# Optimization experiments

Measured on AMD Instinct MI355X. Metric: run time of the kernel, lower is better.

The kernel has to match this reference:

```python
import jax, jax.numpy as jnp
import numpy as np

B = 1024      # batch
D = 512       # input/output dim per module
H = 1024      # expert hidden dim
T = 8         # num_tasks
NTE = 2       # experts per task
NSE = 2       # shared experts
E = T * NTE + NSE   # 18 experts per layer
# expert_input_idx: each expert reads the module it belongs to (tasks 0..7, shared=8)
EXPERT_IDX = np.array([m for m in range(T + 1) for _ in range(2)])  # [E]


def _lin_init(k, shape, fan_in):
    s = 1.0 / np.sqrt(fan_in)
    return jax.random.uniform(k, shape, jnp.float32, -s, s)


def setup_inputs() -> dict:
    key = jax.random.key(0)
    ks = jax.random.split(key, 20)
    inp = {"inputs": jax.random.normal(ks[0], (B, T + 1, D), jnp.float32)}
    # layer 0: experts D->H->D (stacked over E), gates for M=9 modules
    inp["W1_0"] = _lin_init(ks[1], (E, D, H), D)
    inp["b1_0"] = _lin_init(ks[2], (E, H), D)
    inp["W2_0"] = _lin_init(ks[3], (E, H, D), H)
    inp["b2_0"] = _lin_init(ks[4], (E, D), H)
    inp["Wg_0"] = _lin_init(ks[5], (T + 1, D, E), D)
    inp["bg_0"] = _lin_init(ks[6], (T + 1, E), D)
    # layer 1 (final): gates only for M=T modules
    inp["W1_1"] = _lin_init(ks[7], (E, D, H), D)
    inp["b1_1"] = _lin_init(ks[8], (E, H), D)
    inp["W2_1"] = _lin_init(ks[9], (E, H, D), H)
    inp["b2_1"] = _lin_init(ks[10], (E, D), H)
    inp["Wg_1"] = _lin_init(ks[11], (T, D, E), D)
    inp["bg_1"] = _lin_init(ks[12], (T, E), D)
    # self-exp residual weights: per task [L=2, NTE], shared [L-1=1, NSE]
    sc = 1.0 / np.sqrt(NTE)
    inp["sew_task"] = jax.random.uniform(ks[13], (T, 2, NTE), jnp.float32, -sc, sc)
    inp["sew_shared"] = jax.random.uniform(ks[14], (1, NSE), jnp.float32, -sc, sc)
    return inp


def _build_add(rows):
    # rows: list of [2]-vectors, one per fully-active module; block-diagonal layout
    M = len(rows)
    add = jnp.zeros((M, E), jnp.float32)
    for m, w in enumerate(rows):
        add = add.at[m, 2 * m:2 * m + 2].set(w)
    return add


def _layer(x, W1, b1, W2, b2, Wg, bg, add):
    # x: [B, M_in, D]; experts share input of their owning module
    xe = x[:, EXPERT_IDX, :]                                   # [B, E, D]
    h = jax.nn.relu(jnp.einsum('bed,edh->beh', xe, W1) + b1)   # [B, E, H]
    eo = jnp.einsum('beh,eho->beo', h, W2) + b2                # [B, E, D]
    M = Wg.shape[0]
    g = jax.nn.softmax(jnp.einsum('bmd,mde->bme', x[:, :M, :], Wg) + bg, axis=-1)
    g = g + add[None]                                          # self-exp residual
    return jnp.einsum('bme,beo->bmo', g, eo)                   # [B, M, D]


def reference(inputs, W1_0, b1_0, W2_0, b2_0, Wg_0, bg_0,
              W1_1, b1_1, W2_1, b2_1, Wg_1, bg_1, sew_task, sew_shared):
    add0 = _build_add([sew_task[t, 0] for t in range(T)] + [sew_shared[0]])  # [T+1, E]
    add1 = _build_add([sew_task[t, 1] for t in range(T)])                    # [T, E]
    x = _layer(inputs, W1_0, b1_0, W2_0, b2_0, Wg_0, bg_0, add0)  # [B, T+1, D]
    x = _layer(x, W1_1, b1_1, W2_1, b2_1, Wg_1, bg_1, add1)       # [B, T, D]
    return x
```

## Files before the change

kernel.cpp:

```cpp
#include <hip/hip_runtime.h>

typedef unsigned short u16;
typedef unsigned int u32;
typedef __attribute__((ext_vector_type(8))) short short8;
typedef __attribute__((ext_vector_type(4))) float floatx4;

#define GLOAD_LDS16(gp, lp)                                                              \
  __builtin_amdgcn_global_load_lds((const __attribute__((address_space(1))) void*)(gp),  \
                                   (__attribute__((address_space(3))) void*)(lp), 16, 0, 0)

__device__ __forceinline__ u16 f2bf(float f) {
  u32 u = __float_as_uint(f);
  u += 0x7fffu + ((u >> 16) & 1u);
  return (u16)(u >> 16);
}

__device__ __forceinline__ void bf8_to_f(const u16* p, float* o) {
  const uint4 v = *(const uint4*)p;
  const u32 a[4] = {v.x, v.y, v.z, v.w};
#pragma unroll
  for (int i = 0; i < 4; i++) {
    o[2 * i]     = __uint_as_float(a[i] << 16);
    o[2 * i + 1] = __uint_as_float(a[i] & 0xffff0000u);
  }
}

__global__ __launch_bounds__(256) void wtrans_kernel(const float* __restrict__ W,
                                                     u16* __restrict__ WT,
                                                     int K, int N) {
  __shared__ float tile[64][65];
  const int t = threadIdx.x;
  const int e = blockIdx.z;
  const int n0 = blockIdx.x * 64;
  const int k0 = blockIdx.y * 64;
  const float* Wp = W + ((size_t)e * K + k0) * N + n0;
  const int r = t >> 4;
  const int c = (t & 15) << 2;
#pragma unroll
  for (int p = 0; p < 4; p++) {
    const int row = r + p * 16;
    const float4 v = *(const float4*)(Wp + (size_t)row * N + c);
    tile[row][c + 0] = v.x; tile[row][c + 1] = v.y;
    tile[row][c + 2] = v.z; tile[row][c + 3] = v.w;
  }
  __syncthreads();
  u16* WTp = WT + ((size_t)e * N + n0) * K + k0;
#pragma unroll
  for (int p = 0; p < 4; p++) {
    const int row = r + p * 16;
    u32 lo = (u32)f2bf(tile[c + 0][row]) | ((u32)f2bf(tile[c + 1][row]) << 16);
    u32 hi = (u32)f2bf(tile[c + 2][row]) | ((u32)f2bf(tile[c + 3][row]) << 16);
    *(uint2*)(WTp + (size_t)row * K + c) = make_uint2(lo, hi);
  }
}

__global__ __launch_bounds__(256) void wgtrans_kernel(const float* __restrict__ Wg,
                                                      u16* __restrict__ WgT, int total) {
  int idx = blockIdx.x * 256 + threadIdx.x;
  if (idx >= total) return;
  int d = idx & 511;
  int r = idx >> 9;
  int e = r % 18;
  int m = r / 18;
  WgT[idx] = f2bf(Wg[((size_t)(m * 512 + d)) * 18 + e]);
}

__global__ __launch_bounds__(256) void cvtbf_kernel(const float* __restrict__ src,
                                                    u16* __restrict__ dst, int n4) {
  int i = blockIdx.x * 256 + threadIdx.x;
  if (i >= n4) return;
  float4 v = ((const float4*)src)[i];
  u32 lo = (u32)f2bf(v.x) | ((u32)f2bf(v.y) << 16);
  u32 hi = (u32)f2bf(v.z) | ((u32)f2bf(v.w) << 16);
  ((uint2*)dst)[i] = make_uint2(lo, hi);
}

template <bool RELU_BF16_OUT>
__global__ __launch_bounds__(256, 3) void gemm_kernel(
    const u16* __restrict__ A, const u16* __restrict__ BT,
    const float* __restrict__ bias, void* __restrict__ Cout,
    int lda, int a_shift, int a_mul, int ldc, int c_mul, int N, int K) {
  __shared__ __align__(16) u16 As[128 * 64];
  __shared__ __align__(16) u16 Bs[128 * 64];

  const int tid = threadIdx.x;
  const int lane = tid & 63;
  const int wave = tid >> 6;
  const int e = blockIdx.y;
  const int mt = blockIdx.x & 7;
  const int nt = blockIdx.x >> 3;
  const int m0 = mt << 7, n0 = nt << 7;

  const u16* Aexp = A + (size_t)((e >> a_shift) * a_mul);
  const u16* Bexp = BT + (size_t)e * (size_t)N * (size_t)K;

  const int colsw = (((lane & 7) ^ ((lane >> 3) & 7)) << 3);
  const u16* aptr[4];
  const u16* bptr[4];
  u16* lA[4];
  u16* lB[4];
#pragma unroll
  for (int i = 0; i < 4; i++) {
    const int cch = wave * 4 + i;
    const int row = cch * 8 + (lane >> 3);
    aptr[i] = Aexp + (size_t)(m0 + row) * lda + colsw;
    bptr[i] = Bexp + (size_t)(n0 + row) * K + colsw;
    lA[i] = As + cch * 512;
    lB[i] = Bs + cch * 512;
  }

  floatx4 acc[4][4];
#pragma unroll
  for (int i = 0; i < 4; i++)
#pragma unroll
    for (int j = 0; j < 4; j++) acc[i][j] = (floatx4){0.f, 0.f, 0.f, 0.f};

  const int wm = (wave & 1) << 6;
  const int wn = (wave >> 1) << 6;
  const int r15 = lane & 15;
  const int quad = lane >> 4;

  int aoff[4], boff[4];
#pragma unroll
  for (int i = 0; i < 4; i++) {
    const int ra = wm + i * 16 + r15;
    aoff[i] = ra * 64 + ((quad ^ (ra & 7)) << 3);
    const int rb = wn + i * 16 + r15;
    boff[i] = rb * 64 + ((quad ^ (rb & 7)) << 3);
  }

  for (int k0 = 0; k0 < K; k0 += 64) {
    __syncthreads();
#pragma unroll
    for (int i = 0; i < 4; i++) GLOAD_LDS16(aptr[i] + k0, lA[i]);
#pragma unroll
    for (int i = 0; i < 4; i++) GLOAD_LDS16(bptr[i] + k0, lB[i]);
    __syncthreads();
#pragma unroll
    for (int s = 0; s < 2; s++) {
      short8 af[4], bfr[4];
#pragma unroll
      for (int i = 0; i < 4; i++) af[i] = *(const short8*)(As + (aoff[i] ^ (s << 5)));
#pragma unroll
      for (int j = 0; j < 4; j++) bfr[j] = *(const short8*)(Bs + (boff[j] ^ (s << 5)));
#pragma unroll
      for (int i = 0; i < 4; i++)
#pragma unroll
        for (int j = 0; j < 4; j++)
          acc[i][j] = __builtin_amdgcn_mfma_f32_16x16x32_bf16(af[i], bfr[j], acc[i][j], 0, 0, 0);
    }
  }

  const int ccol0 = n0 + wn + r15;
  const int crow0 = m0 + wm + quad * 4;
  float bv[4];
#pragma unroll
  for (int j = 0; j < 4; j++) bv[j] = bias[e * N + ccol0 + j * 16];

  if constexpr (RELU_BF16_OUT) {
    u16* Co = (u16*)Cout + (size_t)e * c_mul;
#pragma unroll
    for (int i = 0; i < 4; i++)
#pragma unroll
      for (int r = 0; r < 4; r++) {
        const size_t rowoff = (size_t)(crow0 + i * 16 + r) * ldc;
#pragma unroll
        for (int j = 0; j < 4; j++) {
          float v = acc[i][j][r] + bv[j];
          v = v > 0.f ? v : 0.f;
          Co[rowoff + ccol0 + j * 16] = f2bf(v);
        }
      }
  } else {
    float* Co = (float*)Cout + (size_t)e * c_mul;
#pragma unroll
    for (int i = 0; i < 4; i++)
#pragma unroll
      for (int r = 0; r < 4; r++) {
        const size_t rowoff = (size_t)(crow0 + i * 16 + r) * ldc;
#pragma unroll
        for (int j = 0; j < 4; j++) Co[rowoff + ccol0 + j * 16] = acc[i][j][r] + bv[j];
      }
  }
}

template <int M, int LAYER>
__global__ __launch_bounds__(256) void gating_kernel(
    const u16* __restrict__ xbf, const u16* __restrict__ WgT,
    const float* __restrict__ bg, const float* __restrict__ sew_task,
    const float* __restrict__ sew_shared, float* __restrict__ wsm) {
  const int lane = threadIdx.x & 63;
  const int wave = threadIdx.x >> 6;
  const int m = blockIdx.y;
  const int b0 = blockIdx.x * 8 + wave * 2;

  float xa[8], xb[8];
  bf8_to_f(xbf + (size_t)b0 * 4608 + m * 512 + lane * 8, xa);
  bf8_to_f(xbf + (size_t)(b0 + 1) * 4608 + m * 512 + lane * 8, xb);

  float lg0[18], lg1[18];
#pragma unroll
  for (int e = 0; e < 18; e++) {
    float w[8];
    bf8_to_f(WgT + ((size_t)m * 18 + e) * 512 + lane * 8, w);
    float s0 = 0.f, s1 = 0.f;
#pragma unroll
    for (int i = 0; i < 8; i++) { s0 = fmaf(w[i], xa[i], s0); s1 = fmaf(w[i], xb[i], s1); }
#pragma unroll
    for (int off = 1; off < 64; off <<= 1) {
      s0 += __shfl_xor(s0, off, 64);
      s1 += __shfl_xor(s1, off, 64);
    }
    const float bgv = bg[m * 18 + e];
    lg0[e] = s0 + bgv;
    lg1[e] = s1 + bgv;
  }
  float mx0 = lg0[0], mx1 = lg1[0];
#pragma unroll
  for (int e = 1; e < 18; e++) { mx0 = fmaxf(mx0, lg0[e]); mx1 = fmaxf(mx1, lg1[e]); }
  float sum0 = 0.f, sum1 = 0.f;
#pragma unroll
  for (int e = 0; e < 18; e++) { sum0 += __expf(lg0[e] - mx0); sum1 += __expf(lg1[e] - mx1); }
  float my0 = lg0[0], my1 = lg1[0];
#pragma unroll
  for (int e = 1; e < 18; e++)
    if (lane == e) { my0 = lg0[e]; my1 = lg1[e]; }
  float w0 = __expf(my0 - mx0) / sum0;
  float w1 = __expf(my1 - mx1) / sum1;
  if ((lane >> 1) == m) {
    float add;
    if (M == 9 && m == 8) add = sew_shared[lane & 1];
    else                  add = sew_task[m * 4 + 2 * LAYER + (lane & 1)];
    w0 += add; w1 += add;
  }
  if (lane < 18) {
    wsm[((size_t)b0 * M + m) * 18 + lane] = w0;
    wsm[((size_t)(b0 + 1) * M + m) * 18 + lane] = w1;
  }
}

template <int M, bool BF16OUT>
__global__ __launch_bounds__(256) void wsum_kernel(
    const float* __restrict__ eo, const float* __restrict__ wsm,
    float* __restrict__ outf, u16* __restrict__ outb) {
  __shared__ float ws[2 * M * 18];
  const int t = threadIdx.x;
  const int b0 = blockIdx.x * 2;
  for (int i = t; i < 2 * M * 18; i += 256) ws[i] = wsm[(size_t)b0 * M * 18 + i];
  __syncthreads();
  const int lb = t >> 7;
  const int s = t & 127;
  const int b = b0 + lb;
  const float* eob = eo + (size_t)b * 9216 + s * 4;
  const float* wr = ws + lb * M * 18;

  float4 acc[M];
#pragma unroll
  for (int m = 0; m < M; m++) acc[m] = make_float4(0.f, 0.f, 0.f, 0.f);
#pragma unroll
  for (int e = 0; e < 18; e++) {
    const float4 v = *(const float4*)(eob + e * 512);
#pragma unroll
    for (int m = 0; m < M; m++) {
      const float w = wr[m * 18 + e];
      acc[m].x = fmaf(w, v.x, acc[m].x);
      acc[m].y = fmaf(w, v.y, acc[m].y);
      acc[m].z = fmaf(w, v.z, acc[m].z);
      acc[m].w = fmaf(w, v.w, acc[m].w);
    }
  }
  if constexpr (BF16OUT) {
    u16* ob = outb + (size_t)b * 4608 + s * 4;
#pragma unroll
    for (int m = 0; m < M; m++) {
      u32 lo = (u32)f2bf(acc[m].x) | ((u32)f2bf(acc[m].y) << 16);
      u32 hi = (u32)f2bf(acc[m].z) | ((u32)f2bf(acc[m].w) << 16);
      *(uint2*)(ob + m * 512) = make_uint2(lo, hi);
    }
  } else {
    float* ob = outf + (size_t)b * (M * 512) + s * 4;
#pragma unroll
    for (int m = 0; m < M; m++) *(float4*)(ob + m * 512) = acc[m];
  }
}

extern "C" void kernel_launch(void* const* d_in, const int* in_sizes, int n_in,
                              void* d_out, int out_size, void* d_ws, size_t ws_size,
                              hipStream_t stream) {
  const float* x0   = (const float*)d_in[0];
  const float* W1_0 = (const float*)d_in[1];
  const float* b1_0 = (const float*)d_in[2];
  const float* W2_0 = (const float*)d_in[3];
  const float* b2_0 = (const float*)d_in[4];
  const float* Wg_0 = (const float*)d_in[5];
  const float* bg_0 = (const float*)d_in[6];
  const float* W1_1 = (const float*)d_in[7];
  const float* b1_1 = (const float*)d_in[8];
  const float* W2_1 = (const float*)d_in[9];
  const float* b2_1 = (const float*)d_in[10];
  const float* Wg_1 = (const float*)d_in[11];
  const float* bg_1 = (const float*)d_in[12];
  const float* sewt = (const float*)d_in[13];
  const float* sews = (const float*)d_in[14];
  float* out = (float*)d_out;

  char* p = (char*)d_ws;
  auto take = [&](size_t n) { char* r = p; p += (n + 255) & ~(size_t)255; return r; };
  u16*   x0bf = (u16*)take(4718592ull * 2);
  u16*   W1T0 = (u16*)take(9437184ull * 2);
  u16*   W2T0 = (u16*)take(9437184ull * 2);
  u16*   W1T1 = (u16*)take(9437184ull * 2);
  u16*   W2T1 = (u16*)take(9437184ull * 2);
  u16*   WgT0 = (u16*)take(82944ull * 2);
  u16*   WgT1 = (u16*)take(73728ull * 2);
  u16*   hbf  = (u16*)take(18874368ull * 2);
  float* eo   = (float*)take(9437184ull * 4);
  u16*   x1bf = (u16*)take(4718592ull * 2);
  float* wsm0 = (float*)take(165888ull * 4);
  float* wsm1 = (float*)take(147456ull * 4);

  dim3 blk(256);
  wtrans_kernel<<<dim3(16, 8, 18), blk, 0, stream>>>(W1_0, W1T0, 512, 1024);
  wtrans_kernel<<<dim3(8, 16, 18), blk, 0, stream>>>(W2_0, W2T0, 1024, 512);
  wtrans_kernel<<<dim3(16, 8, 18), blk, 0, stream>>>(W1_1, W1T1, 512, 1024);
  wtrans_kernel<<<dim3(8, 16, 18), blk, 0, stream>>>(W2_1, W2T1, 1024, 512);
  wgtrans_kernel<<<dim3(324), blk, 0, stream>>>(Wg_0, WgT0, 82944);
  wgtrans_kernel<<<dim3(288), blk, 0, stream>>>(Wg_1, WgT1, 73728);
  cvtbf_kernel<<<dim3(4608), blk, 0, stream>>>(x0, x0bf, 1179648);

  gating_kernel<9, 0><<<dim3(128, 9), blk, 0, stream>>>(x0bf, WgT0, bg_0, sewt, sews, wsm0);
  gemm_kernel<true><<<dim3(64, 18), blk, 0, stream>>>(
      x0bf, W1T0, b1_0, (void*)hbf, 4608, 1, 512, 18432, 1024, 1024, 512);
  gemm_kernel<false><<<dim3(32, 18), blk, 0, stream>>>(
      hbf, W2T0, b2_0, (void*)eo, 18432, 0, 1024, 9216, 512, 512, 1024);
  wsum_kernel<9, true><<<dim3(512), blk, 0, stream>>>(eo, wsm0, nullptr, x1bf);

  gating_kernel<8, 1><<<dim3(128, 8), blk, 0, stream>>>(x1bf, WgT1, bg_1, sewt, sews, wsm1);
  gemm_kernel<true><<<dim3(64, 18), blk, 0, stream>>>(
      x1bf, W1T1, b1_1, (void*)hbf, 4608, 1, 512, 18432, 1024, 1024, 512);
  gemm_kernel<false><<<dim3(32, 18), blk, 0, stream>>>(
      hbf, W2T1, b2_1, (void*)eo, 18432, 0, 1024, 9216, 512, 512, 1024);
  wsum_kernel<8, false><<<dim3(512), blk, 0, stream>>>(eo, wsm1, out, nullptr);
}
```

Before: 406.9 us.

## Remap GEMM blocks per XCD for L2 reuse and merge weight-transpose launches

```diff
diff --git a/kernel.cpp b/kernel.cpp
--- a/kernel.cpp
+++ b/kernel.cpp
@@ -25,14 +25,24 @@
   }
 }
 
-__global__ __launch_bounds__(256) void wtrans_kernel(const float* __restrict__ W,
-                                                     u16* __restrict__ WT,
-                                                     int K, int N) {
+__global__ __launch_bounds__(256) void wtrans4_kernel(
+    const float* __restrict__ W1a, const float* __restrict__ W2a,
+    const float* __restrict__ W1b, const float* __restrict__ W2b,
+    u16* __restrict__ T1a, u16* __restrict__ T2a,
+    u16* __restrict__ T1b, u16* __restrict__ T2b) {
+  const int z = blockIdx.z;
+  const int tsel = z / 18;
+  const int e = z % 18;
+  const int K = (tsel & 1) ? 1024 : 512;
+  const int N = (tsel & 1) ? 512 : 1024;
+  const int n0 = blockIdx.x * 64;
+  const int k0 = blockIdx.y * 64;
+  if (n0 >= N || k0 >= K) return;
+  const float* W = (tsel == 0) ? W1a : (tsel == 1) ? W2a : (tsel == 2) ? W1b : W2b;
+  u16* WT = (tsel == 0) ? T1a : (tsel == 1) ? T2a : (tsel == 2) ? T1b : T2b;
+
   __shared__ float tile[64][65];
   const int t = threadIdx.x;
-  const int e = blockIdx.z;
-  const int n0 = blockIdx.x * 64;
-  const int k0 = blockIdx.y * 64;
   const float* Wp = W + ((size_t)e * K + k0) * N + n0;
   const int r = t >> 4;
   const int c = (t & 15) << 2;
@@ -54,10 +64,18 @@
   }
 }
 
-__global__ __launch_bounds__(256) void wgtrans_kernel(const float* __restrict__ Wg,
-                                                      u16* __restrict__ WgT, int total) {
+__global__ __launch_bounds__(256) void wgtrans_kernel(const float* __restrict__ Wg0,
+                                                      const float* __restrict__ Wg1,
+                                                      u16* __restrict__ WgT0,
+                                                      u16* __restrict__ WgT1) {
   int idx = blockIdx.x * 256 + threadIdx.x;
-  if (idx >= total) return;
+  const float* Wg = Wg0;
+  u16* WgT = WgT0;
+  if (idx >= 82944) {
+    idx -= 82944;
+    if (idx >= 73728) return;
+    Wg = Wg1; WgT = WgT1;
+  }
   int d = idx & 511;
   int r = idx >> 9;
   int e = r % 18;
@@ -79,16 +97,21 @@
 __global__ __launch_bounds__(256, 3) void gemm_kernel(
     const u16* __restrict__ A, const u16* __restrict__ BT,
     const float* __restrict__ bias, void* __restrict__ Cout,
-    int lda, int a_shift, int a_mul, int ldc, int c_mul, int N, int K) {
+    int lda, int a_shift, int a_mul, int ldc, int c_mul, int N, int K, int nshift) {
   __shared__ __align__(16) u16 As[128 * 64];
   __shared__ __align__(16) u16 Bs[128 * 64];
 
   const int tid = threadIdx.x;
   const int lane = tid & 63;
   const int wave = tid >> 6;
-  const int e = blockIdx.y;
-  const int mt = blockIdx.x & 7;
-  const int nt = blockIdx.x >> 3;
+
+  const int L = blockIdx.x;
+  const int per_xcd = gridDim.x >> 3;
+  const int g = (L & 7) * per_xcd + (L >> 3);
+  const int e = g >> nshift;
+  const int wb = g & ((1 << nshift) - 1);
+  const int mt = wb & 7;
+  const int nt = wb >> 3;
   const int m0 = mt << 7, n0 = nt << 7;
 
   const u16* Aexp = A + (size_t)((e >> a_shift) * a_mul);
@@ -320,25 +343,22 @@
   float* wsm1 = (float*)take(147456ull * 4);
 
   dim3 blk(256);
-  wtrans_kernel<<<dim3(16, 8, 18), blk, 0, stream>>>(W1_0, W1T0, 512, 1024);
-  wtrans_kernel<<<dim3(8, 16, 18), blk, 0, stream>>>(W2_0, W2T0, 1024, 512);
-  wtrans_kernel<<<dim3(16, 8, 18), blk, 0, stream>>>(W1_1, W1T1, 512, 1024);
-  wtrans_kernel<<<dim3(8, 16, 18), blk, 0, stream>>>(W2_1, W2T1, 1024, 512);
-  wgtrans_kernel<<<dim3(324), blk, 0, stream>>>(Wg_0, WgT0, 82944);
-  wgtrans_kernel<<<dim3(288), blk, 0, stream>>>(Wg_1, WgT1, 73728);
+  wtrans4_kernel<<<dim3(16, 16, 72), blk, 0, stream>>>(W1_0, W2_0, W1_1, W2_1,
+                                                       W1T0, W2T0, W1T1, W2T1);
+  wgtrans_kernel<<<dim3(613), blk, 0, stream>>>(Wg_0, Wg_1, WgT0, WgT1);
   cvtbf_kernel<<<dim3(4608), blk, 0, stream>>>(x0, x0bf, 1179648);
 
   gating_kernel<9, 0><<<dim3(128, 9), blk, 0, stream>>>(x0bf, WgT0, bg_0, sewt, sews, wsm0);
-  gemm_kernel<true><<<dim3(64, 18), blk, 0, stream>>>(
-      x0bf, W1T0, b1_0, (void*)hbf, 4608, 1, 512, 18432, 1024, 1024, 512);
-  gemm_kernel<false><<<dim3(32, 18), blk, 0, stream>>>(
-      hbf, W2T0, b2_0, (void*)eo, 18432, 0, 1024, 9216, 512, 512, 1024);
+  gemm_kernel<true><<<dim3(1152), blk, 0, stream>>>(
+      x0bf, W1T0, b1_0, (void*)hbf, 4608, 1, 512, 18432, 1024, 1024, 512, 6);
+  gemm_kernel<false><<<dim3(576), blk, 0, stream>>>(
+      hbf, W2T0, b2_0, (void*)eo, 18432, 0, 1024, 9216, 512, 512, 1024, 5);
   wsum_kernel<9, true><<<dim3(512), blk, 0, stream>>>(eo, wsm0, nullptr, x1bf);
 
   gating_kernel<8, 1><<<dim3(128, 8), blk, 0, stream>>>(x1bf, WgT1, bg_1, sewt, sews, wsm1);
-  gemm_kernel<true><<<dim3(64, 18), blk, 0, stream>>>(
-      x1bf, W1T1, b1_1, (void*)hbf, 4608, 1, 512, 18432, 1024, 1024, 512);
-  gemm_kernel<false><<<dim3(32, 18), blk, 0, stream>>>(
-      hbf, W2T1, b2_1, (void*)eo, 18432, 0, 1024, 9216, 512, 512, 1024);
+  gemm_kernel<true><<<dim3(1152), blk, 0, stream>>>(
+      x1bf, W1T1, b1_1, (void*)hbf, 4608, 1, 512, 18432, 1024, 1024, 512, 6);
+  gemm_kernel<false><<<dim3(576), blk, 0, stream>>>(
+      hbf, W2T1, b2_1, (void*)eo, 18432, 0, 1024, 9216, 512, 512, 1024, 5);
   wsum_kernel<8, false><<<dim3(512), blk, 0, stream>>>(eo, wsm1, out, nullptr);
 }
```

Result: faster. 392.5 us (-3.5%).
